# Kernel optimization log

Hardware: AMD Instinct MI355X
Metric: run time of the kernel (lower is better)

## Reference

```python
import jax, jax.numpy as jnp
import numpy as np

D_MODEL = 768
N_HEAD = 12

def setup_inputs() -> dict:
    key = jax.random.key(0)
    ks = jax.random.split(key, 5)
    B, T, C = 2, 2048, D_MODEL
    s = 1.0 / np.sqrt(C)
    x = jax.random.normal(ks[0], (B, T, C), dtype=jnp.float32)
    W_attn = jax.random.normal(ks[1], (C, 3 * C), dtype=jnp.float32) * s
    b_attn = jnp.zeros((3 * C,), dtype=jnp.float32)
    W_proj = jax.random.normal(ks[2], (C, C), dtype=jnp.float32) * s
    b_proj = jnp.zeros((C,), dtype=jnp.float32)
    return {"x": x, "W_attn": W_attn, "b_attn": b_attn, "W_proj": W_proj, "b_proj": b_proj}

def reference(x, W_attn, b_attn, W_proj, b_proj):
    B, T, C = x.shape
    H, Dh = N_HEAD, C // N_HEAD
    qkv = x @ W_attn + b_attn  # [B,T,3C]
    q, k, v = jnp.split(qkv, 3, axis=-1)
    q = q.reshape(B, T, H, Dh).transpose(0, 2, 1, 3)  # [B,H,T,Dh]
    k = k.reshape(B, T, H, Dh).transpose(0, 2, 1, 3)
    v = v.reshape(B, T, H, Dh).transpose(0, 2, 1, 3)
    att = jnp.einsum('bhqd,bhkd->bhqk', q, k) * (1.0 / np.sqrt(Dh))
    mask = jnp.tril(jnp.ones((T, T), dtype=bool))  # causal
    att = jnp.where(mask, att, -jnp.inf)
    att = jax.nn.softmax(att, axis=-1)
    y = jnp.einsum('bhqk,bhkd->bhqd', att, v)
    y = y.transpose(0, 2, 1, 3).reshape(B, T, C)
    return y @ W_proj + b_proj
```

## Files before the change

kernel.cpp:

```cpp
#include <hip/hip_runtime.h>
#include <hip/hip_bf16.h>
#include <math.h>

#define BB 2
#define TT 2048
#define CC 768
#define HH 12
#define DD 64
#define KD 768
#define NCH 40

#define QSCALE 0.18033688011112044f
#define THR2 11.5f

typedef __attribute__((ext_vector_type(8))) short bf16x8;
typedef __attribute__((ext_vector_type(4))) float f32x4;
typedef __attribute__((ext_vector_type(4))) float f32x4v;
typedef __attribute__((ext_vector_type(4))) ushort u16x4;

static __device__ __forceinline__ ushort f2bf(float f) {
  union { float f; unsigned u; } v; v.f = f;
  unsigned r = v.u + 0x7FFF + ((v.u >> 16) & 1);
  return (ushort)(r >> 16);
}
static __device__ __forceinline__ float bf2f(ushort u) {
  union { unsigned u; float f; } v; v.u = ((unsigned)u) << 16;
  return v.f;
}

#define NB_CVT 3072
#define NB_TA  1728
#define NB_TP  576

__global__ __launch_bounds__(256) void prep_fused(
    const float* __restrict__ x, ushort* __restrict__ xb,
    const float* __restrict__ Wa, ushort* __restrict__ Wat,
    const float* __restrict__ Wp, ushort* __restrict__ Wpt) {
  const int bid = blockIdx.x;
  const int tid = threadIdx.x;
  if (bid < NB_CVT) {
    const int i = bid * 256 + tid;
    f32x4v v = ((const f32x4v*)x)[i];
    u16x4 o;
    o.x = f2bf(v.x); o.y = f2bf(v.y); o.z = f2bf(v.z); o.w = f2bf(v.w);
    ((u16x4*)xb)[i] = o;
    return;
  }
  __shared__ float t[32][33];
  const float* W; ushort* Wt; int N, idx;
  if (bid < NB_CVT + NB_TA) { W = Wa; Wt = Wat; N = 3 * CC; idx = bid - NB_CVT; }
  else                      { W = Wp; Wt = Wpt; N = CC;     idx = bid - NB_CVT - NB_TA; }
  const int ntx = N / 32;
  const int n0 = (idx % ntx) * 32, k0 = (idx / ntx) * 32;
  const int tx = tid & 31, ty = tid >> 5;
#pragma unroll
  for (int j = 0; j < 32; j += 8)
    t[ty + j][tx] = W[(size_t)(k0 + ty + j) * N + n0 + tx];
  __syncthreads();
#pragma unroll
  for (int j = 0; j < 32; j += 8)
    Wt[(size_t)(n0 + ty + j) * KD + k0 + tx] = f2bf(t[tx][ty + j]);
}

__global__ __launch_bounds__(256) void gemm_mfma(
    const ushort* __restrict__ A, const ushort* __restrict__ Bt,
    const float* __restrict__ bias, int N, int mode,
    ushort* __restrict__ Qo, ushort* __restrict__ Ko, ushort* __restrict__ Vo,
    float* __restrict__ Of) {
  __shared__ ushort As[128 * 32];
  __shared__ ushort Bs[128 * 32];
  const int tid = threadIdx.x;
  const int w = tid >> 6, lane = tid & 63;
  const int wr = w >> 1, wc = w & 1;
  const int grp = lane >> 4, colk = lane & 15;
  const int bm = blockIdx.y * 128, bn = blockIdx.x * 128;

  f32x4 acc[4][4] = {};

  auto* AsL = (__attribute__((address_space(3))) char*)As;
  auto* BsL = (__attribute__((address_space(3))) char*)Bs;

  for (int k0 = 0; k0 < KD; k0 += 32) {
#pragma unroll
    for (int i = 0; i < 2; ++i) {
      const int idx = tid + i * 256;
      const int row = idx >> 2, g = idx & 3;
      const int eoff = (g * 8) ^ ((row & 3) << 3);
      const ushort* sa = A + (size_t)(bm + row) * KD + k0 + eoff;
      const ushort* sb = Bt + (size_t)(bn + row) * KD + k0 + eoff;
      __builtin_amdgcn_global_load_lds(
          (const __attribute__((address_space(1))) void*)sa,
          (__attribute__((address_space(3))) void*)(AsL + w * 1024 + i * 4096), 16, 0, 0);
      __builtin_amdgcn_global_load_lds(
          (const __attribute__((address_space(1))) void*)sb,
          (__attribute__((address_space(3))) void*)(BsL + w * 1024 + i * 4096), 16, 0, 0);
    }
    __syncthreads();

    bf16x8 af[4], bf[4];
    const int sw = (colk & 3) << 3;
#pragma unroll
    for (int m = 0; m < 4; ++m)
      af[m] = *(const bf16x8*)&As[(wr * 64 + m * 16 + colk) * 32 + ((grp * 8) ^ sw)];
#pragma unroll
    for (int n = 0; n < 4; ++n)
      bf[n] = *(const bf16x8*)&Bs[(wc * 64 + n * 16 + colk) * 32 + ((grp * 8) ^ sw)];
#pragma unroll
    for (int m = 0; m < 4; ++m)
#pragma unroll
      for (int n = 0; n < 4; ++n)
        acc[m][n] = __builtin_amdgcn_mfma_f32_16x16x32_bf16(af[m], bf[n], acc[m][n], 0, 0, 0);
    __syncthreads();
  }

#pragma unroll
  for (int m = 0; m < 4; ++m) {
    const int gro = bm + wr * 64 + m * 16 + grp * 4;
#pragma unroll
    for (int n = 0; n < 4; ++n) {
      const int col = bn + wc * 64 + n * 16 + colk;
      const float bv = bias[col];
#pragma unroll
      for (int j = 0; j < 4; ++j) {
        const int row = gro + j;
        float v = acc[m][n][j] + bv;
        if (mode == 0) {
          const int which = col / CC;
          const int c = col - which * CC;
          const int hh = c >> 6, d = c & 63;
          const int b = row >> 11, t = row & 2047;
          if (which == 0) v *= QSCALE;
          const ushort bvv = f2bf(v);
          if (which == 0)
            Qo[((size_t)((b * HH + hh) * TT + t)) * DD + d] = bvv;
          else if (which == 1)
            Ko[((size_t)((b * HH + hh) * TT + t)) * DD + d] = bvv;
          else
            Vo[((size_t)((b * HH + hh) * DD + d)) * TT + t] = bvv;
        } else {
          Of[(size_t)row * N + col] = v;
        }
      }
    }
  }
}

__global__ __launch_bounds__(512, 4) void attn_mfma(
    const ushort* __restrict__ Q, const ushort* __restrict__ K,
    const ushort* __restrict__ Vt, ushort* __restrict__ Po,
    float* __restrict__ Pml) {
  const int c = NCH - 1 - (int)blockIdx.x;
  int qq, ci;
  if (c < 4)       { qq = c;                               ci = 0; }
  else if (c < 12) { int o_ = c - 4;  qq = 4  + (o_ >> 1); ci = o_ & 1; }
  else if (c < 24) { int o_ = c - 12; qq = 8  + o_ / 3;    ci = o_ % 3; }
  else             { int o_ = c - 24; qq = 12 + (o_ >> 2); ci = o_ & 3; }
  const int h = blockIdx.y, b = blockIdx.z;
  const int bh = b * HH + h;
  const size_t hb = (size_t)bh * TT * DD;
  const int kbase = ci * 512;
  const int nt = min(8, 2 * (qq + 1) - ci * 8);

  __shared__ ushort Ks[64][72];
  __shared__ ushort Vs[64][72];
  __shared__ ushort Ps[8][16][72];
  __shared__ float scw[8][16];

  const int tid = threadIdx.x;
  const int w = tid >> 6, lane = tid & 63;
  const int grp = lane >> 4, colk = lane & 15;
  const int q0w = qq * 128 + w * 16;
  const int qme = q0w + colk;

  const ushort* Kg = K + hb;
  const ushort* Vg = Vt + hb;

  bf16x8 qf[2];
  {
    const ushort* qp = Q + hb + (size_t)(q0w + colk) * DD + 8 * grp;
    qf[0] = *(const bf16x8*)(qp);
    qf[1] = *(const bf16x8*)(qp + 32);
  }

  f32x4 o[4] = {};
  float m = -1e30f, l = 0.f;

  const int srow = tid >> 3;
  const int scol = (tid & 7) * 8;

  {
    bf16x8 k0a = *(const bf16x8*)&Kg[(size_t)(kbase + srow) * DD + scol];
    bf16x8 v0a = *(const bf16x8*)&Vg[(size_t)srow * TT + kbase + scol];
    *(bf16x8*)&Ks[srow][scol] = k0a;
    *(bf16x8*)&Vs[srow][scol] = v0a;
  }
  __syncthreads();

  for (int it = 0; it < nt; ++it) {
    const int k0 = kbase + it * 64;
    const bool pfn = (it + 1 < nt);
    bf16x8 nk0, nv0;
    if (pfn) {
      nk0 = *(const bf16x8*)&Kg[(size_t)(k0 + 64 + srow) * DD + scol];
      nv0 = *(const bf16x8*)&Vg[(size_t)srow * TT + k0 + 64 + scol];
    }

    if (k0 <= q0w) {
      f32x4 s2[4] = {};
      __builtin_amdgcn_s_setprio(1);
#pragma unroll
      for (int kb = 0; kb < 4; ++kb) {
        bf16x8 kf0 = *(const bf16x8*)&Ks[16 * kb + colk][8 * grp];
        bf16x8 kf1 = *(const bf16x8*)&Ks[16 * kb + colk][32 + 8 * grp];
        s2[kb] = __builtin_amdgcn_mfma_f32_16x16x32_bf16(kf0, qf[0], s2[kb], 0, 0, 0);
        s2[kb] = __builtin_amdgcn_mfma_f32_16x16x32_bf16(kf1, qf[1], s2[kb], 0, 0, 0);
      }
      __builtin_amdgcn_s_setprio(0);

      if (k0 + 63 > q0w) {
#pragma unroll
        for (int kb = 0; kb < 4; ++kb)
#pragma unroll
          for (int r = 0; r < 4; ++r)
            if (k0 + 16 * kb + 4 * grp + r > qme) s2[kb][r] = -1e30f;
      }
      float pm = -1e30f;
#pragma unroll
      for (int kb = 0; kb < 4; ++kb)
        pm = fmaxf(pm, fmaxf(fmaxf(s2[kb][0], s2[kb][1]), fmaxf(s2[kb][2], s2[kb][3])));
      pm = fmaxf(pm, __shfl_xor(pm, 16));
      pm = fmaxf(pm, __shfl_xor(pm, 32));

      if (__any(pm > m + THR2)) {
        const float mn = fmaxf(m, pm);
        const float sc = exp2f(m - mn);
        m = mn;
        l *= sc;
        if (grp == 0) scw[w][colk] = sc;
        const f32x4 s4 = *(const f32x4*)&scw[w][4 * grp];
#pragma unroll
        for (int n = 0; n < 4; ++n)
#pragma unroll
          for (int r = 0; r < 4; ++r) o[n][r] *= s4[r];
      }

      float ps = 0.f;
#pragma unroll
      for (int kb = 0; kb < 4; ++kb) {
        const float p0 = exp2f(s2[kb][0] - m);
        const float p1 = exp2f(s2[kb][1] - m);
        const float p2 = exp2f(s2[kb][2] - m);
        const float p3 = exp2f(s2[kb][3] - m);
        ps += (p0 + p1) + (p2 + p3);
        union { __hip_bfloat162 h2[2]; uint2 u2; } pk;
        pk.h2[0] = __float22bfloat162_rn(make_float2(p0, p1));
        pk.h2[1] = __float22bfloat162_rn(make_float2(p2, p3));
        *(uint2*)&Ps[w][colk][16 * kb + 4 * grp] = pk.u2;
      }
      ps += __shfl_xor(ps, 16);
      ps += __shfl_xor(ps, 32);
      l += ps;

      bf16x8 pf0 = *(const bf16x8*)&Ps[w][colk][8 * grp];
      bf16x8 pf1 = *(const bf16x8*)&Ps[w][colk][32 + 8 * grp];
      __builtin_amdgcn_s_setprio(1);
#pragma unroll
      for (int n = 0; n < 4; ++n) {
        bf16x8 vf0 = *(const bf16x8*)&Vs[16 * n + colk][8 * grp];
        bf16x8 vf1 = *(const bf16x8*)&Vs[16 * n + colk][32 + 8 * grp];
        o[n] = __builtin_amdgcn_mfma_f32_16x16x32_bf16(pf0, vf0, o[n], 0, 0, 0);
        o[n] = __builtin_amdgcn_mfma_f32_16x16x32_bf16(pf1, vf1, o[n], 0, 0, 0);
      }
      __builtin_amdgcn_s_setprio(0);
    }

    if (pfn) {
      __syncthreads();
      *(bf16x8*)&Ks[srow][scol] = nk0;
      *(bf16x8*)&Vs[srow][scol] = nv0;
      __syncthreads();
    }
  }

  const size_t pbase = ((size_t)bh * NCH + c) * 128;
#pragma unroll
  for (int r = 0; r < 4; ++r) {
    const int row = w * 16 + grp * 4 + r;
#pragma unroll
    for (int n = 0; n < 4; ++n)
      Po[(pbase + row) * 64 + 16 * n + colk] = f2bf(o[n][r]);
  }
  if (grp == 0) {
    const int row = w * 16 + colk;
    Pml[(pbase + row) * 2] = m;
    Pml[(pbase + row) * 2 + 1] = l;
  }
}

__global__ __launch_bounds__(256) void attn_merge(
    const ushort* __restrict__ Po, const float* __restrict__ Pml,
    ushort* __restrict__ Yb) {
  const int qq = blockIdx.x, h = blockIdx.y, b = blockIdx.z;
  const int bh = b * HH + h;
  const int qh = qq >> 1;
  const int gg = qh >> 2;
  const int nch = gg + 1;
  const int gb = (gg == 0) ? 0 : (gg == 1) ? 4 : (gg == 2) ? 12 : 24;
  const int cb = gb + nch * (qh - 4 * gg);
  const int rowo = (qq & 1) * 64;

  const int tid = threadIdx.x;
  const int row = tid >> 2;
  const int d0 = (tid & 3) * 16;

  float mi[4], li[4];
  float M = -1e30f;
#pragma unroll
  for (int i = 0; i < 4; ++i) {
    if (i < nch) {
      const size_t pb = ((size_t)bh * NCH + cb + i) * 128 + rowo + row;
      mi[i] = Pml[pb * 2];
      li[i] = Pml[pb * 2 + 1];
      M = fmaxf(M, mi[i]);
    }
  }
  float acc[16] = {};
  float lt = 0.f;
#pragma unroll
  for (int i = 0; i < 4; ++i) {
    if (i < nch) {
      const float wgt = exp2f(mi[i] - M);
      lt += li[i] * wgt;
      const ushort* pp = Po + (((size_t)bh * NCH + cb + i) * 128 + rowo + row) * 64 + d0;
      bf16x8 a = *(const bf16x8*)pp;
      bf16x8 bv = *(const bf16x8*)(pp + 8);
#pragma unroll
      for (int j = 0; j < 8; ++j) {
        acc[j] += wgt * bf2f((ushort)a[j]);
        acc[8 + j] += wgt * bf2f((ushort)bv[j]);
      }
    }
  }
  const float inv = 1.0f / lt;
  const int t = qq * 64 + row;
  ushort* yp = Yb + ((size_t)(b * TT) + t) * CC + h * DD + d0;
  bf16x8 o0, o1;
#pragma unroll
  for (int j = 0; j < 8; ++j) {
    o0[j] = (short)f2bf(acc[j] * inv);
    o1[j] = (short)f2bf(acc[8 + j] * inv);
  }
  *(bf16x8*)yp = o0;
  *(bf16x8*)(yp + 8) = o1;
}

extern "C" void kernel_launch(void* const* d_in, const int* in_sizes, int n_in,
                              void* d_out, int out_size, void* d_ws, size_t ws_size,
                              hipStream_t stream) {
  const float* x      = (const float*)d_in[0];
  const float* W_attn = (const float*)d_in[1];
  const float* b_attn = (const float*)d_in[2];
  const float* W_proj = (const float*)d_in[3];
  const float* b_proj = (const float*)d_in[4];
  float* out = (float*)d_out;

  const size_t per = (size_t)BB * TT * CC;
  ushort* Q   = (ushort*)d_ws;
  ushort* K   = Q + per;
  ushort* VtT = K + per;
  ushort* Yb  = VtT + per;
  ushort* Wpt = Yb + per;
  ushort* xb  = Wpt + (size_t)CC * CC;
  ushort* Wat = xb + per;
  ushort* Po  = xb;
  float*  Pml = (float*)(Po + (size_t)BB * HH * NCH * 128 * 64);

  prep_fused<<<dim3(NB_CVT + NB_TA + NB_TP), 256, 0, stream>>>(
      x, xb, W_attn, Wat, W_proj, Wpt);

  gemm_mfma<<<dim3(3 * CC / 128, BB * TT / 128), 256, 0, stream>>>(
      xb, Wat, b_attn, 3 * CC, 0, Q, K, VtT, nullptr);
  attn_mfma<<<dim3(NCH, HH, BB), 512, 0, stream>>>(Q, K, VtT, Po, Pml);
  attn_merge<<<dim3(TT / 64, HH, BB), 256, 0, stream>>>(Po, Pml, Yb);
  gemm_mfma<<<dim3(CC / 128, BB * TT / 128), 256, 0, stream>>>(
      Yb, Wpt, b_proj, CC, 1, nullptr, nullptr, nullptr, out);
}
```

Baseline: 116.5 us.

## Process two 16-row query tiles per wave in attention to reuse K/V fragments

The attention kernel moves from 8 waves of 16 query rows each to 4 waves of 32 rows, handled as two interleaved 16-row sub-tiles (A and B). Each K and V fragment read from LDS now feeds two MFMAs, which halves LDS fragment traffic per unit of compute and gives the scheduler independent MFMA chains to interleave. Softmax is factored into a macro applied to each sub-tile in turn, and the P staging buffer is reused between them. In exchange, register pressure roughly doubles, each block has half as many waves, and the causal skip test now works at 32-row granularity, so slightly more masked work is done near the diagonal.

New measurement: 122.6 us. +5.2%, slower.

```diff
diff --git a/kernel.cpp b/kernel.cpp
--- a/kernel.cpp
+++ b/kernel.cpp
@@ -145,7 +145,53 @@
   }
 }
 
-__global__ __launch_bounds__(512, 4) void attn_mfma(
+#define SOFTMAX_SET(S2, M, L, O, QME, MASKQ)                                  \
+  do {                                                                        \
+    if (k0 + 63 > (MASKQ)) {                                                  \
+      _Pragma("unroll")                                                       \
+      for (int kb = 0; kb < 4; ++kb)                                          \
+        _Pragma("unroll")                                                     \
+        for (int r = 0; r < 4; ++r)                                           \
+          if (k0 + 16 * kb + 4 * grp + r > (QME)) S2[kb][r] = -1e30f;         \
+    }                                                                         \
+    float pm = -1e30f;                                                        \
+    _Pragma("unroll")                                                         \
+    for (int kb = 0; kb < 4; ++kb)                                            \
+      pm = fmaxf(pm, fmaxf(fmaxf(S2[kb][0], S2[kb][1]),                       \
+                           fmaxf(S2[kb][2], S2[kb][3])));                     \
+    pm = fmaxf(pm, __shfl_xor(pm, 16));                                       \
+    pm = fmaxf(pm, __shfl_xor(pm, 32));                                       \
+    if (__any(pm > (M) + THR2)) {                                             \
+      const float mn = fmaxf((M), pm);                                        \
+      const float sc = exp2f((M) - mn);                                       \
+      (M) = mn;                                                               \
+      (L) *= sc;                                                              \
+      if (grp == 0) scw[w][colk] = sc;                                        \
+      const f32x4 s4 = *(const f32x4*)&scw[w][4 * grp];                       \
+      _Pragma("unroll")                                                       \
+      for (int n = 0; n < 4; ++n)                                             \
+        _Pragma("unroll")                                                     \
+        for (int r = 0; r < 4; ++r) O[n][r] *= s4[r];                         \
+    }                                                                         \
+    float ps = 0.f;                                                           \
+    _Pragma("unroll")                                                         \
+    for (int kb = 0; kb < 4; ++kb) {                                          \
+      const float p0 = exp2f(S2[kb][0] - (M));                                \
+      const float p1 = exp2f(S2[kb][1] - (M));                                \
+      const float p2 = exp2f(S2[kb][2] - (M));                                \
+      const float p3 = exp2f(S2[kb][3] - (M));                                \
+      ps += (p0 + p1) + (p2 + p3);                                            \
+      union { __hip_bfloat162 h2[2]; uint2 u2; } pk;                          \
+      pk.h2[0] = __float22bfloat162_rn(make_float2(p0, p1));                  \
+      pk.h2[1] = __float22bfloat162_rn(make_float2(p2, p3));                  \
+      *(uint2*)&Ps[w][colk][16 * kb + 4 * grp] = pk.u2;                       \
+    }                                                                         \
+    ps += __shfl_xor(ps, 16);                                                 \
+    ps += __shfl_xor(ps, 32);                                                 \
+    (L) += ps;                                                                \
+  } while (0)
+
+__global__ __launch_bounds__(256, 3) void attn_mfma(
     const ushort* __restrict__ Q, const ushort* __restrict__ K,
     const ushort* __restrict__ Vt, ushort* __restrict__ Po,
     float* __restrict__ Pml) {
@@ -163,113 +209,89 @@
 
   __shared__ ushort Ks[64][72];
   __shared__ ushort Vs[64][72];
-  __shared__ ushort Ps[8][16][72];
-  __shared__ float scw[8][16];
+  __shared__ ushort Ps[4][16][72];
+  __shared__ float scw[4][16];
 
   const int tid = threadIdx.x;
   const int w = tid >> 6, lane = tid & 63;
   const int grp = lane >> 4, colk = lane & 15;
-  const int q0w = qq * 128 + w * 16;
-  const int qme = q0w + colk;
+  const int q0w = qq * 128 + w * 32;
+  const int qmeA = q0w + colk;
+  const int qmeB = q0w + 16 + colk;
 
   const ushort* Kg = K + hb;
   const ushort* Vg = Vt + hb;
 
-  bf16x8 qf[2];
+  bf16x8 qfA[2], qfB[2];
   {
-    const ushort* qp = Q + hb + (size_t)(q0w + colk) * DD + 8 * grp;
-    qf[0] = *(const bf16x8*)(qp);
-    qf[1] = *(const bf16x8*)(qp + 32);
-  }
-
-  f32x4 o[4] = {};
-  float m = -1e30f, l = 0.f;
-
-  const int srow = tid >> 3;
-  const int scol = (tid & 7) * 8;
+    const ushort* qpA = Q + hb + (size_t)qmeA * DD + 8 * grp;
+    qfA[0] = *(const bf16x8*)(qpA);
+    qfA[1] = *(const bf16x8*)(qpA + 32);
+    const ushort* qpB = Q + hb + (size_t)qmeB * DD + 8 * grp;
+    qfB[0] = *(const bf16x8*)(qpB);
+    qfB[1] = *(const bf16x8*)(qpB + 32);
+  }
+
+  f32x4 oA[4] = {}, oB[4] = {};
+  float mA = -1e30f, lA = 0.f, mB = -1e30f, lB = 0.f;
+
+  const int srow = tid >> 2;
+  const int scol = (tid & 3) * 16;
 
   {
     bf16x8 k0a = *(const bf16x8*)&Kg[(size_t)(kbase + srow) * DD + scol];
+    bf16x8 k0b = *(const bf16x8*)&Kg[(size_t)(kbase + srow) * DD + scol + 8];
     bf16x8 v0a = *(const bf16x8*)&Vg[(size_t)srow * TT + kbase + scol];
+    bf16x8 v0b = *(const bf16x8*)&Vg[(size_t)srow * TT + kbase + scol + 8];
     *(bf16x8*)&Ks[srow][scol] = k0a;
+    *(bf16x8*)&Ks[srow][scol + 8] = k0b;
     *(bf16x8*)&Vs[srow][scol] = v0a;
+    *(bf16x8*)&Vs[srow][scol + 8] = v0b;
   }
   __syncthreads();
 
   for (int it = 0; it < nt; ++it) {
     const int k0 = kbase + it * 64;
     const bool pfn = (it + 1 < nt);
-    bf16x8 nk0, nv0;
+    bf16x8 nk0, nk1, nv0, nv1;
     if (pfn) {
       nk0 = *(const bf16x8*)&Kg[(size_t)(k0 + 64 + srow) * DD + scol];
+      nk1 = *(const bf16x8*)&Kg[(size_t)(k0 + 64 + srow) * DD + scol + 8];
       nv0 = *(const bf16x8*)&Vg[(size_t)srow * TT + k0 + 64 + scol];
+      nv1 = *(const bf16x8*)&Vg[(size_t)srow * TT + k0 + 64 + scol + 8];
     }
 
     if (k0 <= q0w) {
-      f32x4 s2[4] = {};
+      f32x4 sA[4] = {}, sB[4] = {};
       __builtin_amdgcn_s_setprio(1);
 #pragma unroll
       for (int kb = 0; kb < 4; ++kb) {
         bf16x8 kf0 = *(const bf16x8*)&Ks[16 * kb + colk][8 * grp];
         bf16x8 kf1 = *(const bf16x8*)&Ks[16 * kb + colk][32 + 8 * grp];
-        s2[kb] = __builtin_amdgcn_mfma_f32_16x16x32_bf16(kf0, qf[0], s2[kb], 0, 0, 0);
-        s2[kb] = __builtin_amdgcn_mfma_f32_16x16x32_bf16(kf1, qf[1], s2[kb], 0, 0, 0);
+        sA[kb] = __builtin_amdgcn_mfma_f32_16x16x32_bf16(kf0, qfA[0], sA[kb], 0, 0, 0);
+        sB[kb] = __builtin_amdgcn_mfma_f32_16x16x32_bf16(kf0, qfB[0], sB[kb], 0, 0, 0);
+        sA[kb] = __builtin_amdgcn_mfma_f32_16x16x32_bf16(kf1, qfA[1], sA[kb], 0, 0, 0);
+        sB[kb] = __builtin_amdgcn_mfma_f32_16x16x32_bf16(kf1, qfB[1], sB[kb], 0, 0, 0);
       }
       __builtin_amdgcn_s_setprio(0);
 
-      if (k0 + 63 > q0w) {
-#pragma unroll
-        for (int kb = 0; kb < 4; ++kb)
-#pragma unroll
-          for (int r = 0; r < 4; ++r)
-            if (k0 + 16 * kb + 4 * grp + r > qme) s2[kb][r] = -1e30f;
-      }
-      float pm = -1e30f;
-#pragma unroll
-      for (int kb = 0; kb < 4; ++kb)
-        pm = fmaxf(pm, fmaxf(fmaxf(s2[kb][0], s2[kb][1]), fmaxf(s2[kb][2], s2[kb][3])));
-      pm = fmaxf(pm, __shfl_xor(pm, 16));
-      pm = fmaxf(pm, __shfl_xor(pm, 32));
-
-      if (__any(pm > m + THR2)) {
-        const float mn = fmaxf(m, pm);
-        const float sc = exp2f(m - mn);
-        m = mn;
-        l *= sc;
-        if (grp == 0) scw[w][colk] = sc;
-        const f32x4 s4 = *(const f32x4*)&scw[w][4 * grp];
-#pragma unroll
-        for (int n = 0; n < 4; ++n)
-#pragma unroll
-          for (int r = 0; r < 4; ++r) o[n][r] *= s4[r];
-      }
-
-      float ps = 0.f;
-#pragma unroll
-      for (int kb = 0; kb < 4; ++kb) {
-        const float p0 = exp2f(s2[kb][0] - m);
-        const float p1 = exp2f(s2[kb][1] - m);
-        const float p2 = exp2f(s2[kb][2] - m);
-        const float p3 = exp2f(s2[kb][3] - m);
-        ps += (p0 + p1) + (p2 + p3);
-        union { __hip_bfloat162 h2[2]; uint2 u2; } pk;
-        pk.h2[0] = __float22bfloat162_rn(make_float2(p0, p1));
-        pk.h2[1] = __float22bfloat162_rn(make_float2(p2, p3));
-        *(uint2*)&Ps[w][colk][16 * kb + 4 * grp] = pk.u2;
-      }
-      ps += __shfl_xor(ps, 16);
-      ps += __shfl_xor(ps, 32);
-      l += ps;
-
-      bf16x8 pf0 = *(const bf16x8*)&Ps[w][colk][8 * grp];
-      bf16x8 pf1 = *(const bf16x8*)&Ps[w][colk][32 + 8 * grp];
+      SOFTMAX_SET(sA, mA, lA, oA, qmeA, q0w);
+      bf16x8 pfA0 = *(const bf16x8*)&Ps[w][colk][8 * grp];
+      bf16x8 pfA1 = *(const bf16x8*)&Ps[w][colk][32 + 8 * grp];
+
+      SOFTMAX_SET(sB, mB, lB, oB, qmeB, q0w + 16);
+      bf16x8 pfB0 = *(const bf16x8*)&Ps[w][colk][8 * grp];
+      bf16x8 pfB1 = *(const bf16x8*)&Ps[w][colk][32 + 8 * grp];
+
       __builtin_amdgcn_s_setprio(1);
 #pragma unroll
       for (int n = 0; n < 4; ++n) {
         bf16x8 vf0 = *(const bf16x8*)&Vs[16 * n + colk][8 * grp];
         bf16x8 vf1 = *(const bf16x8*)&Vs[16 * n + colk][32 + 8 * grp];
-        o[n] = __builtin_amdgcn_mfma_f32_16x16x32_bf16(pf0, vf0, o[n], 0, 0, 0);
-        o[n] = __builtin_amdgcn_mfma_f32_16x16x32_bf16(pf1, vf1, o[n], 0, 0, 0);
+        oA[n] = __builtin_amdgcn_mfma_f32_16x16x32_bf16(pfA0, vf0, oA[n], 0, 0, 0);
+        oB[n] = __builtin_amdgcn_mfma_f32_16x16x32_bf16(pfB0, vf0, oB[n], 0, 0, 0);
+        oA[n] = __builtin_amdgcn_mfma_f32_16x16x32_bf16(pfA1, vf1, oA[n], 0, 0, 0);
+        oB[n] = __builtin_amdgcn_mfma_f32_16x16x32_bf16(pfB1, vf1, oB[n], 0, 0, 0);
       }
       __builtin_amdgcn_s_setprio(0);
     }
@@ -277,7 +299,9 @@
     if (pfn) {
       __syncthreads();
       *(bf16x8*)&Ks[srow][scol] = nk0;
+      *(bf16x8*)&Ks[srow][scol + 8] = nk1;
       *(bf16x8*)&Vs[srow][scol] = nv0;
+      *(bf16x8*)&Vs[srow][scol + 8] = nv1;
       __syncthreads();
     }
   }
@@ -285,15 +309,20 @@
   const size_t pbase = ((size_t)bh * NCH + c) * 128;
 #pragma unroll
   for (int r = 0; r < 4; ++r) {
-    const int row = w * 16 + grp * 4 + r;
-#pragma unroll
-    for (int n = 0; n < 4; ++n)
-      Po[(pbase + row) * 64 + 16 * n + colk] = f2bf(o[n][r]);
+    const int rowA = w * 32 + grp * 4 + r;
+    const int rowB = rowA + 16;
+#pragma unroll
+    for (int n = 0; n < 4; ++n) {
+      Po[(pbase + rowA) * 64 + 16 * n + colk] = f2bf(oA[n][r]);
+      Po[(pbase + rowB) * 64 + 16 * n + colk] = f2bf(oB[n][r]);
+    }
   }
   if (grp == 0) {
-    const int row = w * 16 + colk;
-    Pml[(pbase + row) * 2] = m;
-    Pml[(pbase + row) * 2 + 1] = l;
+    const int rowA = w * 32 + colk;
+    Pml[(pbase + rowA) * 2] = mA;
+    Pml[(pbase + rowA) * 2 + 1] = lA;
+    Pml[(pbase + rowA + 16) * 2] = mB;
+    Pml[(pbase + rowA + 16) * 2 + 1] = lB;
   }
 }
 
@@ -380,7 +409,7 @@
 
   gemm_mfma<<<dim3(3 * CC / 128, BB * TT / 128), 256, 0, stream>>>(
       xb, Wat, b_attn, 3 * CC, 0, Q, K, VtT, nullptr);
-  attn_mfma<<<dim3(NCH, HH, BB), 512, 0, stream>>>(Q, K, VtT, Po, Pml);
+  attn_mfma<<<dim3(NCH, HH, BB), 256, 0, stream>>>(Q, K, VtT, Po, Pml);
   attn_merge<<<dim3(TT / 64, HH, BB), 256, 0, stream>>>(Po, Pml, Yb);
   gemm_mfma<<<dim3(CC / 128, BB * TT / 128), 256, 0, stream>>>(
       Yb, Wpt, b_proj, CC, 1, nullptr, nullptr, nullptr, out);
```
